# Kernel tuning notes

Hardware: AMD Instinct MI355X
Metric: run time of the kernel (lower is better)

## Reference

```python
import jax, jax.numpy as jnp
import numpy as np

KQ_DIM = 132  # latent_dim == kq_dim so gather covers full rows
EPS = 1e-12


def setup_inputs() -> dict:
    key = jax.random.key(0)
    ks = jax.random.split(key, 8)
    B, C, H, W = 8, 3, 128, 128
    N, K, D = 2048, 32, KQ_DIM
    indices = jax.random.randint(ks[0], (3, B, N, K), 0, H * W + 1, dtype=jnp.int32)
    img = jax.random.normal(ks[1], (B, C, H, W), dtype=jnp.float32)
    # stand-in backbone: 3x3 conv (ResidualDenseNetwork not in source)
    conv_w = jax.random.normal(ks[2], (D, C, 3, 3), dtype=jnp.float32) * (1.0 / np.sqrt(C * 9))
    conv_b = jnp.zeros((D,), dtype=jnp.float32)
    sc = 1.0 / np.sqrt(D)
    ks_w = jax.random.normal(ks[3], (D, D), dtype=jnp.float32) * sc
    ks_b = jax.random.normal(ks[4], (D,), dtype=jnp.float32) * sc
    qs_w = jax.random.normal(ks[5], (D, D), dtype=jnp.float32) * sc
    qs_b = jax.random.normal(ks[6], (D,), dtype=jnp.float32) * sc
    return {"indices": indices, "img": img, "conv_w": conv_w, "conv_b": conv_b,
            "ks_w": ks_w, "ks_b": ks_b, "qs_w": qs_w, "qs_b": qs_b}


def reference(indices, img, conv_w, conv_b, ks_w, ks_b, qs_w, qs_b):
    _, B, N, K = indices.shape
    # backbone conv: [B, D, H, W]
    feat = jax.lax.conv_general_dilated(
        img, conv_w, window_strides=(1, 1), padding='SAME',
        dimension_numbers=('NCHW', 'OIHW', 'NCHW')) + conv_b[None, :, None, None]
    # torch F.normalize(dim=-1) BEFORE permute -> L2 over last spatial (width) axis
    norm = jnp.linalg.norm(feat, axis=-1, keepdims=True)
    feat = feat / jnp.maximum(norm, EPS)
    # permute(0,2,3,1): [B, H, W, D] -> flatten spatial
    feat = jnp.transpose(feat, (0, 2, 3, 1))
    Bf, Hh, Ww, D = feat.shape
    flat = feat.reshape(Bf, Hh * Ww, D)
    flat = jnp.concatenate([flat, jnp.zeros((Bf, 1, D), dtype=flat.dtype)], axis=1)
    flat_ks = flat @ ks_w.T + ks_b  # [B, WH+1, D]
    flat_qs = flat @ qs_w.T + qs_b
    x_idx = indices[1].reshape(B, N * K)  # [B, N*K]
    y_idx = indices[2].reshape(B, N * K)
    x_feat = jnp.take_along_axis(flat_ks, x_idx[:, :, None], axis=1).reshape(B, N, K, D)
    y_feat = jnp.take_along_axis(flat_qs, y_idx[:, :, None], axis=1).reshape(B, N, K, D)
    # entailment logits: scaled dot product over feature dim
    logits = (x_feat * y_feat).sum(axis=-1) * (D ** -0.5)  # [B, N, K]
    return logits
```

## Files before the change

kernel.cpp:

```cpp
#include <hip/hip_runtime.h>
#include <hip/hip_bf16.h>
#include <math.h>

#define B_ 8
#define H_ 128
#define W_ 128
#define C_ 3
#define D_ 132
#define HW_ (H_*W_)
#define RPB_ (HW_+1)
#define NROWS_ (B_*RPB_)
#define AROWS_ 131136
#define FSTRIDE_ 136
#define MSTRIDE_ 168
#define MROWS_ 136
#define MELEMS_ (MROWS_*MSTRIDE_)
#define MALLOC_ 23040
#define NK_ 65536
#define NOUT_ (B_*NK_)

typedef __attribute__((ext_vector_type(8))) short short8v;
typedef __attribute__((ext_vector_type(8))) unsigned short ushort8v;
typedef __attribute__((ext_vector_type(4))) float f32x4;

#define GLOAD16(gp, lp) __builtin_amdgcn_global_load_lds( \
  (const __attribute__((address_space(1))) unsigned int*)(gp), \
  (__attribute__((address_space(3))) unsigned int*)(void*)(lp), 16, 0, 0)

__device__ inline float bf2f(unsigned short u) {
  return __uint_as_float(((unsigned)u) << 16);
}
__device__ inline unsigned short f2bf(float f) {
  __hip_bfloat16 hb = __float2bfloat16(f);
  return *(unsigned short*)&hb;
}

__global__ __launch_bounds__(512) void prep_kernel(
    const float* __restrict__ ks_w, const float* __restrict__ ks_b,
    const float* __restrict__ qs_w, const float* __restrict__ qs_b,
    unsigned short* __restrict__ Mb, float* __restrict__ cc) {
  int idx = blockIdx.x * 512 + threadIdx.x;
  if (idx >= MALLOC_) return;
  float val = 0.f;
  if (idx < MELEMS_) {
    int a = idx / MSTRIDE_;
    int k = idx - a * MSTRIDE_;
    if (k < D_) {
      if (a < D_) {
        for (int o = 0; o < D_; ++o)
          val = fmaf(ks_w[o * D_ + a], qs_w[o * D_ + k], val);
      } else if (a == 132) {
        for (int o = 0; o < D_; ++o)
          val = fmaf(qs_b[o], ks_w[o * D_ + k], val);
      } else if (a == 133) {
        for (int o = 0; o < D_; ++o)
          val = fmaf(ks_b[o], qs_w[o * D_ + k], val);
      }
    }
  }
  Mb[idx] = f2bf(val);
  if (idx == 0) {
    float s = 0.f;
    for (int o = 0; o < D_; ++o) s = fmaf(ks_b[o], qs_b[o], s);
    cc[0] = s;
  }
}

__device__ __forceinline__ float conv_item16(
    const float* __restrict__ in_s, const float* __restrict__ w_s,
    float bias, int d, int w0, float* acc) {
  float wt[27];
#pragma unroll
  for (int j = 0; j < 27; ++j) wt[j] = w_s[d * 27 + j];
#pragma unroll
  for (int i = 0; i < 16; ++i) acc[i] = bias;
#pragma unroll
  for (int ck = 0; ck < 9; ++ck) {
    const float4* p4 = (const float4*)(in_s + ck * 132);
    float v[20];
#pragma unroll
    for (int j = 0; j < 5; ++j) {
      float4 t4 = p4[(w0 >> 2) + j];
      v[4 * j + 0] = t4.x; v[4 * j + 1] = t4.y;
      v[4 * j + 2] = t4.z; v[4 * j + 3] = t4.w;
    }
#pragma unroll
    for (int i = 0; i < 16; ++i) {
      float a0 = fmaf(v[i], wt[ck * 3 + 0], acc[i]);
      float a1 = fmaf(v[i + 1], wt[ck * 3 + 1], a0);
      acc[i] = fmaf(v[i + 2], wt[ck * 3 + 2], a1);
    }
  }
  float ssq = 0.f;
#pragma unroll
  for (int i = 0; i < 16; ++i) ssq = fmaf(acc[i], acc[i], ssq);
  return ssq;
}

__global__ __launch_bounds__(512, 4) void fused_conv_gemm_kernel(
    const float* __restrict__ img, const float* __restrict__ cw,
    const float* __restrict__ cb, unsigned short* __restrict__ fb,
    const unsigned short* __restrict__ Mb, const float* __restrict__ cc,
    unsigned short* __restrict__ zb) {
  int bid = blockIdx.x;
  int tid = threadIdx.x;

  if (bid == B_ * H_) {
    float cval = cc[0];
    for (int i = tid; i < B_ * FSTRIDE_; i += 512) {
      int b = i / FSTRIDE_, d = i - (i / FSTRIDE_) * FSTRIDE_;
      size_t r = (size_t)b * RPB_ + HW_;
      fb[r * FSTRIDE_ + d] = (d == 132) ? 0x3F80 : 0;
      unsigned short zv = 0;
      if (d == 132) zv = f2bf(cval);
      else if (d == 133) zv = 0x3F80;
      zb[r * FSTRIDE_ + d] = zv;
    }
    return;
  }

  int wave = tid >> 6, lane = tid & 63;
  __shared__ __align__(16) unsigned short Ms[MALLOC_];
  __shared__ float nscale[132];
  __shared__ __align__(16) char un[34880];
  float* in_s = (float*)un;
  float* w_s  = in_s + 9 * 132;
  float* b_s  = w_s + 132 * 27;
  float* parts = b_s + 132;
  unsigned short* As = (unsigned short*)un;

  for (int ch = wave; ch < 45; ch += 8)
    GLOAD16(Mb + (size_t)ch * 512 + lane * 8, Ms + ch * 512);

  int b = bid >> 7, h = bid & 127;
  for (int i = tid; i < 9 * 132; i += 512) {
    int ck = i / 132, x = i - ck * 132;
    int c = ck / 3, kh = ck - c * 3;
    int hh = h + kh - 1, ww = x - 1;
    float val = 0.f;
    if (x >= 1 && x <= 128 && hh >= 0 && hh < H_)
      val = img[((size_t)(b * C_ + c) * H_ + hh) * W_ + ww];
    in_s[i] = val;
  }
  for (int i = tid; i < D_ * 27; i += 512) w_s[i] = cw[i];
  if (tid < D_) b_s[tid] = cb[tid];
  __syncthreads();

  float acc0[16], acc1[16], acc2[16];
  int i0 = tid, i1 = tid + 512;
  int wg0 = i0 / 132, dd0 = i0 - wg0 * 132;
  int wg1 = i1 / 132, dd1 = i1 - wg1 * 132;
  parts[wg0 * 132 + dd0] = conv_item16(in_s, w_s, b_s[dd0], dd0, wg0 * 16, acc0);
  parts[wg1 * 132 + dd1] = conv_item16(in_s, w_s, b_s[dd1], dd1, wg1 * 16, acc1);
  int dd2 = 0;
  if (tid < 32) {
    dd2 = 100 + tid;
    parts[7 * 132 + dd2] = conv_item16(in_s, w_s, b_s[dd2], dd2, 112, acc2);
  }
  __syncthreads();
  if (tid < 132) {
    float s = 0.f;
#pragma unroll
    for (int rr = 0; rr < 8; ++rr) s += parts[rr * 132 + tid];
    nscale[tid] = 1.f / fmaxf(sqrtf(s), 1e-12f);
  }
  __syncthreads();

  {
    float sc = nscale[dd0];
#pragma unroll
    for (int i = 0; i < 16; ++i)
      As[(wg0 * 16 + i) * FSTRIDE_ + dd0] = f2bf(acc0[i] * sc);
    sc = nscale[dd1];
#pragma unroll
    for (int i = 0; i < 16; ++i)
      As[(wg1 * 16 + i) * FSTRIDE_ + dd1] = f2bf(acc1[i] * sc);
  }
  if (tid < 32) {
    float sc = nscale[dd2];
#pragma unroll
    for (int i = 0; i < 16; ++i)
      As[(112 + i) * FSTRIDE_ + dd2] = f2bf(acc2[i] * sc);
  }
  if (tid < 128) {
    uint2 tv; tv.x = 0x3F80u; tv.y = 0u;
    *(uint2*)&As[tid * FSTRIDE_ + 132] = tv;
  }
  if (tid < 32) As[128 * FSTRIDE_ + tid] = 0;
  __syncthreads();

  size_t rowbase = (size_t)b * RPB_ + (size_t)h * W_;
  unsigned short* fbase = fb + rowbase * FSTRIDE_;
  for (int i2 = tid; i2 < 2176; i2 += 512)
    *(ushort8v*)(fbase + i2 * 8) = *(const ushort8v*)(As + i2 * 8);

  int c15 = lane & 15, kg = lane >> 4;
  const unsigned short* arow = As + (wave * 16 + c15) * FSTRIDE_ + kg * 8;
  const unsigned short* brow = Ms + c15 * MSTRIDE_ + kg * 8;
  f32x4 acc[9] = {};
#pragma unroll
  for (int ks = 0; ks < 5; ++ks) {
    short8v af = *(const short8v*)(arow + ks * 32);
#pragma unroll
    for (int ct = 0; ct < 9; ++ct) {
      short8v bf = *(const short8v*)(brow + ct * 16 * MSTRIDE_ + ks * 32);
      acc[ct] = __builtin_amdgcn_mfma_f32_16x16x32_bf16(af, bf, acc[ct], 0, 0, 0);
    }
  }
  __syncthreads();

  float cval = cc[0];
  int r0 = wave * 16 + kg * 4;
#pragma unroll
  for (int ct = 0; ct < 9; ++ct) {
    int col = ct * 16 + c15;
#pragma unroll
    for (int j = 0; j < 4; ++j) {
      int r = r0 + j;
      if (col < D_)            As[r * FSTRIDE_ + col] = f2bf(acc[ct][j]);
      else if (col == 132)     fb[(rowbase + r) * FSTRIDE_ + 133] = f2bf(acc[ct][j]);
      else if (col == 133)     As[r * FSTRIDE_ + 132] = f2bf(acc[ct][j] + cval);
      else if (col == 134)     As[r * FSTRIDE_ + 133] = 0x3F80;
      else if (col == 135)     As[r * FSTRIDE_ + 134] = 0;
      else if (col == 136)     As[r * FSTRIDE_ + 135] = 0;
    }
  }
  __syncthreads();

  unsigned short* zbase = zb + rowbase * FSTRIDE_;
  for (int i2 = tid; i2 < 2176; i2 += 512)
    *(ushort8v*)(zbase + i2 * 8) = *(const ushort8v*)(As + i2 * 8);
}

__global__ __launch_bounds__(256) void gather_kernel(
    const int* __restrict__ xi, const int* __restrict__ yi,
    const unsigned short* __restrict__ flat, const unsigned short* __restrict__ zb,
    float* __restrict__ out) {
  const float scale = 0.08703882797784892f;
  int bi = blockIdx.x;
  int b = bi & 7;
  int chunk = bi >> 3;
  int lane = threadIdx.x & 7;
  int rem1 = chunk * 32 + (threadIdx.x >> 3);
  int rem2 = rem1 + 32768;

  size_t ib1 = (size_t)b * NK_ + rem1;
  size_t ib2 = (size_t)b * NK_ + rem2;
  int x1 = xi[ib1], y1 = yi[ib1];
  int x2 = xi[ib2], y2 = yi[ib2];
  size_t bbase = (size_t)b * RPB_;
  const unsigned short* fx1 = flat + (bbase + x1) * FSTRIDE_;
  const unsigned short* zy1 = zb + (bbase + y1) * FSTRIDE_;
  const unsigned short* fx2 = flat + (bbase + x2) * FSTRIDE_;
  const unsigned short* zy2 = zb + (bbase + y2) * FSTRIDE_;

  int e0 = lane * 8, e1 = 64 + lane * 8;
  ushort8v a10 = *(const ushort8v*)(fx1 + e0);
  ushort8v a11 = *(const ushort8v*)(fx1 + e1);
  ushort8v z10 = *(const ushort8v*)(zy1 + e0);
  ushort8v z11 = *(const ushort8v*)(zy1 + e1);
  ushort8v a20 = *(const ushort8v*)(fx2 + e0);
  ushort8v a21 = *(const ushort8v*)(fx2 + e1);
  ushort8v z20 = *(const ushort8v*)(zy2 + e0);
  ushort8v z21 = *(const ushort8v*)(zy2 + e1);

  float acc1 = 0.f, acc2 = 0.f;
#pragma unroll
  for (int t = 0; t < 8; ++t) {
    acc1 = fmaf(bf2f(a10[t]), bf2f(z10[t]), acc1);
    acc2 = fmaf(bf2f(a20[t]), bf2f(z20[t]), acc2);
  }
#pragma unroll
  for (int t = 0; t < 8; ++t) {
    acc1 = fmaf(bf2f(a11[t]), bf2f(z11[t]), acc1);
    acc2 = fmaf(bf2f(a21[t]), bf2f(z21[t]), acc2);
  }
  if (lane == 0) {
    ushort8v a1t = *(const ushort8v*)(fx1 + 128);
    ushort8v z1t = *(const ushort8v*)(zy1 + 128);
    ushort8v a2t = *(const ushort8v*)(fx2 + 128);
    ushort8v z2t = *(const ushort8v*)(zy2 + 128);
#pragma unroll
    for (int t = 0; t < 8; ++t) {
      acc1 = fmaf(bf2f(a1t[t]), bf2f(z1t[t]), acc1);
      acc2 = fmaf(bf2f(a2t[t]), bf2f(z2t[t]), acc2);
    }
  }
  acc1 += __shfl_xor(acc1, 1);
  acc2 += __shfl_xor(acc2, 1);
  acc1 += __shfl_xor(acc1, 2);
  acc2 += __shfl_xor(acc2, 2);
  acc1 += __shfl_xor(acc1, 4);
  acc2 += __shfl_xor(acc2, 4);
  if (lane == 0) {
    out[((size_t)b << 16) | rem1] = acc1 * scale;
    out[((size_t)b << 16) | rem2] = acc2 * scale;
  }
}

extern "C" void kernel_launch(void* const* d_in, const int* in_sizes, int n_in,
                              void* d_out, int out_size, void* d_ws, size_t ws_size,
                              hipStream_t stream) {
  const int* indices  = (const int*)d_in[0];
  const float* img    = (const float*)d_in[1];
  const float* conv_w = (const float*)d_in[2];
  const float* conv_b = (const float*)d_in[3];
  const float* ks_w   = (const float*)d_in[4];
  const float* ks_b   = (const float*)d_in[5];
  const float* qs_w   = (const float*)d_in[6];
  const float* qs_b   = (const float*)d_in[7];
  float* out = (float*)d_out;

  char* w = (char*)d_ws;
  unsigned short* flatb = (unsigned short*)w;
  size_t off = (size_t)AROWS_ * FSTRIDE_ * 2;
  unsigned short* zbuf = (unsigned short*)(w + off); off += (size_t)AROWS_ * FSTRIDE_ * 2;
  unsigned short* Mb = (unsigned short*)(w + off);   off += MALLOC_ * 2;
  float* cc = (float*)(w + off);

  const int* xi = indices + (size_t)B_ * NK_;
  const int* yi = indices + (size_t)2 * B_ * NK_;

  hipLaunchKernelGGL(prep_kernel, dim3(MALLOC_ / 512), dim3(512), 0, stream,
                     ks_w, ks_b, qs_w, qs_b, Mb, cc);
  hipLaunchKernelGGL(fused_conv_gemm_kernel, dim3(B_ * H_ + 1), dim3(512), 0, stream,
                     img, conv_w, conv_b, flatb, Mb, cc, zbuf);
  hipLaunchKernelGGL(gather_kernel, dim3(NOUT_ / 64), dim3(256), 0, stream,
                     xi, yi, flatb, zbuf, out);
}
```

Baseline: 87.72 us.

## Split feature rows into 256-byte main block and separate 16-byte tail array

```diff
diff --git a/kernel.cpp b/kernel.cpp
--- a/kernel.cpp
+++ b/kernel.cpp
@@ -99,35 +99,41 @@
 
 __global__ __launch_bounds__(512, 4) void fused_conv_gemm_kernel(
     const float* __restrict__ img, const float* __restrict__ cw,
-    const float* __restrict__ cb, unsigned short* __restrict__ fb,
-    const unsigned short* __restrict__ Mb, const float* __restrict__ cc,
-    unsigned short* __restrict__ zb) {
+    const float* __restrict__ cb, unsigned short* __restrict__ fmain,
+    unsigned short* __restrict__ ft, const unsigned short* __restrict__ Mb,
+    const float* __restrict__ cc, unsigned short* __restrict__ zmain,
+    unsigned short* __restrict__ zt) {
   int bid = blockIdx.x;
   int tid = threadIdx.x;
 
   if (bid == B_ * H_) {
     float cval = cc[0];
-    for (int i = tid; i < B_ * FSTRIDE_; i += 512) {
-      int b = i / FSTRIDE_, d = i - (i / FSTRIDE_) * FSTRIDE_;
+    for (int i = tid; i < B_ * 128; i += 512) {
+      int b = i >> 7, c = i & 127;
       size_t r = (size_t)b * RPB_ + HW_;
-      fb[r * FSTRIDE_ + d] = (d == 132) ? 0x3F80 : 0;
-      unsigned short zv = 0;
-      if (d == 132) zv = f2bf(cval);
-      else if (d == 133) zv = 0x3F80;
-      zb[r * FSTRIDE_ + d] = zv;
+      fmain[r * 128 + c] = 0;
+      zmain[r * 128 + c] = 0;
+    }
+    if (tid < B_) {
+      size_t r = (size_t)tid * RPB_ + HW_;
+      ushort8v f8 = {0, 0, 0, 0, 0x3F80, 0, 0, 0};
+      *(ushort8v*)(ft + r * 8) = f8;
+      ushort8v z8 = {0, 0, 0, 0, f2bf(cval), 0x3F80, 0, 0};
+      *(ushort8v*)(zt + r * 8) = z8;
     }
     return;
   }
 
   int wave = tid >> 6, lane = tid & 63;
   __shared__ __align__(16) unsigned short Ms[MALLOC_];
-  __shared__ float nscale[132];
+  __shared__ __align__(16) float nscale[132];
   __shared__ __align__(16) char un[34880];
   float* in_s = (float*)un;
   float* w_s  = in_s + 9 * 132;
   float* b_s  = w_s + 132 * 27;
   float* parts = b_s + 132;
   unsigned short* As = (unsigned short*)un;
+  unsigned short* su_s = (unsigned short*)nscale;
 
   for (int ch = wave; ch < 45; ch += 8)
     GLOAD16(Mb + (size_t)ch * 512 + lane * 8, Ms + ch * 512);
@@ -190,9 +196,13 @@
   __syncthreads();
 
   size_t rowbase = (size_t)b * RPB_ + (size_t)h * W_;
-  unsigned short* fbase = fb + rowbase * FSTRIDE_;
-  for (int i2 = tid; i2 < 2176; i2 += 512)
-    *(ushort8v*)(fbase + i2 * 8) = *(const ushort8v*)(As + i2 * 8);
+  unsigned short* fmb = fmain + rowbase * 128;
+  for (int i2 = tid; i2 < 2048; i2 += 512) {
+    int r = i2 >> 4, c8 = i2 & 15;
+    *(ushort8v*)(fmb + r * 128 + c8 * 8) = *(const ushort8v*)(As + r * FSTRIDE_ + c8 * 8);
+  }
+  uint2 ftl = {0, 0};
+  if (tid < 128) ftl = *(const uint2*)&As[tid * FSTRIDE_ + 128];
 
   int c15 = lane & 15, kg = lane >> 4;
   const unsigned short* arow = As + (wave * 16 + c15) * FSTRIDE_ + kg * 8;
@@ -218,7 +228,7 @@
     for (int j = 0; j < 4; ++j) {
       int r = r0 + j;
       if (col < D_)            As[r * FSTRIDE_ + col] = f2bf(acc[ct][j]);
-      else if (col == 132)     fb[(rowbase + r) * FSTRIDE_ + 133] = f2bf(acc[ct][j]);
+      else if (col == 132)     su_s[r] = f2bf(acc[ct][j]);
       else if (col == 133)     As[r * FSTRIDE_ + 132] = f2bf(acc[ct][j] + cval);
       else if (col == 134)     As[r * FSTRIDE_ + 133] = 0x3F80;
       else if (col == 135)     As[r * FSTRIDE_ + 134] = 0;
@@ -227,14 +237,30 @@
   }
   __syncthreads();
 
-  unsigned short* zbase = zb + rowbase * FSTRIDE_;
-  for (int i2 = tid; i2 < 2176; i2 += 512)
-    *(ushort8v*)(zbase + i2 * 8) = *(const ushort8v*)(As + i2 * 8);
+  unsigned short* zmb = zmain + rowbase * 128;
+  for (int i2 = tid; i2 < 2048; i2 += 512) {
+    int r = i2 >> 4, c8 = i2 & 15;
+    *(ushort8v*)(zmb + r * 128 + c8 * 8) = *(const ushort8v*)(As + r * FSTRIDE_ + c8 * 8);
+  }
+  if (tid < 128) {
+    *(ushort8v*)(zt + (rowbase + tid) * 8) = *(const ushort8v*)(As + tid * FSTRIDE_ + 128);
+    ushort8v f8;
+    f8[0] = (unsigned short)(ftl.x & 0xFFFFu);
+    f8[1] = (unsigned short)(ftl.x >> 16);
+    f8[2] = (unsigned short)(ftl.y & 0xFFFFu);
+    f8[3] = (unsigned short)(ftl.y >> 16);
+    f8[4] = 0x3F80;
+    f8[5] = su_s[tid];
+    f8[6] = 0;
+    f8[7] = 0;
+    *(ushort8v*)(ft + (rowbase + tid) * 8) = f8;
+  }
 }
 
 __global__ __launch_bounds__(256) void gather_kernel(
     const int* __restrict__ xi, const int* __restrict__ yi,
-    const unsigned short* __restrict__ flat, const unsigned short* __restrict__ zb,
+    const unsigned short* __restrict__ fmain, const unsigned short* __restrict__ ft,
+    const unsigned short* __restrict__ zmain, const unsigned short* __restrict__ zt,
     float* __restrict__ out) {
   const float scale = 0.08703882797784892f;
   int bi = blockIdx.x;
@@ -249,20 +275,27 @@
   int x1 = xi[ib1], y1 = yi[ib1];
   int x2 = xi[ib2], y2 = yi[ib2];
   size_t bbase = (size_t)b * RPB_;
-  const unsigned short* fx1 = flat + (bbase + x1) * FSTRIDE_;
-  const unsigned short* zy1 = zb + (bbase + y1) * FSTRIDE_;
-  const unsigned short* fx2 = flat + (bbase + x2) * FSTRIDE_;
-  const unsigned short* zy2 = zb + (bbase + y2) * FSTRIDE_;
-
-  int e0 = lane * 8, e1 = 64 + lane * 8;
+  const unsigned short* fx1 = fmain + (bbase + x1) * 128;
+  const unsigned short* zy1 = zmain + (bbase + y1) * 128;
+  const unsigned short* fx2 = fmain + (bbase + x2) * 128;
+  const unsigned short* zy2 = zmain + (bbase + y2) * 128;
+
+  int e0 = lane * 16;
   ushort8v a10 = *(const ushort8v*)(fx1 + e0);
-  ushort8v a11 = *(const ushort8v*)(fx1 + e1);
+  ushort8v a11 = *(const ushort8v*)(fx1 + e0 + 8);
   ushort8v z10 = *(const ushort8v*)(zy1 + e0);
-  ushort8v z11 = *(const ushort8v*)(zy1 + e1);
+  ushort8v z11 = *(const ushort8v*)(zy1 + e0 + 8);
   ushort8v a20 = *(const ushort8v*)(fx2 + e0);
-  ushort8v a21 = *(const ushort8v*)(fx2 + e1);
+  ushort8v a21 = *(const ushort8v*)(fx2 + e0 + 8);
   ushort8v z20 = *(const ushort8v*)(zy2 + e0);
-  ushort8v z21 = *(const ushort8v*)(zy2 + e1);
+  ushort8v z21 = *(const ushort8v*)(zy2 + e0 + 8);
+  ushort8v a1t, z1t, a2t, z2t;
+  if (lane == 0) {
+    a1t = *(const ushort8v*)(ft + (bbase + x1) * 8);
+    z1t = *(const ushort8v*)(zt + (bbase + y1) * 8);
+    a2t = *(const ushort8v*)(ft + (bbase + x2) * 8);
+    z2t = *(const ushort8v*)(zt + (bbase + y2) * 8);
+  }
 
   float acc1 = 0.f, acc2 = 0.f;
 #pragma unroll
@@ -276,10 +309,6 @@
     acc2 = fmaf(bf2f(a21[t]), bf2f(z21[t]), acc2);
   }
   if (lane == 0) {
-    ushort8v a1t = *(const ushort8v*)(fx1 + 128);
-    ushort8v z1t = *(const ushort8v*)(zy1 + 128);
-    ushort8v a2t = *(const ushort8v*)(fx2 + 128);
-    ushort8v z2t = *(const ushort8v*)(zy2 + 128);
 #pragma unroll
     for (int t = 0; t < 8; ++t) {
       acc1 = fmaf(bf2f(a1t[t]), bf2f(z1t[t]), acc1);
@@ -312,10 +341,12 @@
   float* out = (float*)d_out;
 
   char* w = (char*)d_ws;
-  unsigned short* flatb = (unsigned short*)w;
-  size_t off = (size_t)AROWS_ * FSTRIDE_ * 2;
-  unsigned short* zbuf = (unsigned short*)(w + off); off += (size_t)AROWS_ * FSTRIDE_ * 2;
-  unsigned short* Mb = (unsigned short*)(w + off);   off += MALLOC_ * 2;
+  unsigned short* fmain = (unsigned short*)w;
+  size_t off = (size_t)AROWS_ * 128 * 2;
+  unsigned short* zmain = (unsigned short*)(w + off); off += (size_t)AROWS_ * 128 * 2;
+  unsigned short* ftl = (unsigned short*)(w + off);   off += (size_t)AROWS_ * 8 * 2;
+  unsigned short* ztl = (unsigned short*)(w + off);   off += (size_t)AROWS_ * 8 * 2;
+  unsigned short* Mb = (unsigned short*)(w + off);    off += MALLOC_ * 2;
   float* cc = (float*)(w + off);
 
   const int* xi = indices + (size_t)B_ * NK_;
@@ -324,7 +355,7 @@
   hipLaunchKernelGGL(prep_kernel, dim3(MALLOC_ / 512), dim3(512), 0, stream,
                      ks_w, ks_b, qs_w, qs_b, Mb, cc);
   hipLaunchKernelGGL(fused_conv_gemm_kernel, dim3(B_ * H_ + 1), dim3(512), 0, stream,
-                     img, conv_w, conv_b, flatb, Mb, cc, zbuf);
+                     img, conv_w, conv_b, fmain, ftl, Mb, cc, zmain, ztl);
   hipLaunchKernelGGL(gather_kernel, dim3(NOUT_ / 64), dim3(256), 0, stream,
-                     xi, yi, flatb, zbuf, out);
-}
+                     xi, yi, fmain, ftl, zmain, ztl, out);
+}
```

Result: faster. 80.78 us (-7.9%).
